# Kernel optimization log

Hardware: AMD Instinct MI355X
Metric: run time of the kernel (lower is better)

## Reference

```python
import jax, jax.numpy as jnp
import numpy as np

MAX_WORDS = 256  # = batch['labels'].shape[1]


def _align(hidden, word_ids, max_words):
    """Batched segment-mean: (B,S,D) subtoken states -> (B,max_words,D) word states.
    Equivalent to align_subtokens_to_words applied per sample (word_ids all valid)."""
    B, S, D = hidden.shape
    seg = (word_ids.astype(jnp.int32) + jnp.arange(B, dtype=jnp.int32)[:, None] * max_words).reshape(-1)
    sums = jax.ops.segment_sum(hidden.reshape(-1, D), seg, num_segments=B * max_words)
    cnts = jax.ops.segment_sum(jnp.ones((B * S,), hidden.dtype), seg, num_segments=B * max_words)
    out = jnp.where(cnts[:, None] > 0, sums / jnp.maximum(cnts, 1.0)[:, None], 0.0)
    return out.reshape(B, max_words, D)


def setup_inputs() -> dict:
    key = jax.random.key(0)
    ks = jax.random.split(key, 8)
    B, S, D, W = 64, 512, 768, MAX_WORDS
    h_hing_sub = jax.random.normal(ks[0], (B, S, D), dtype=jnp.float32)
    h_rob_sub = jax.random.normal(ks[1], (B, S, D), dtype=jnp.float32)
    hing_word_ids = jnp.sort(jax.random.randint(ks[2], (B, S), 0, W), axis=-1).astype(jnp.int32)
    rob_word_ids = jnp.sort(jax.random.randint(ks[3], (B, S), 0, W), axis=-1).astype(jnp.int32)
    num_words = jax.random.randint(ks[4], (B,), 1, W).astype(jnp.int32)
    router_w1 = jax.random.normal(ks[5], (2 * D, 256), dtype=jnp.float32) * (1.0 / np.sqrt(2 * D))
    router_b1 = jnp.zeros((256,), jnp.float32)
    router_w2 = jax.random.normal(ks[6], (256, 1), dtype=jnp.float32) * (1.0 / 16.0)
    router_b2 = jnp.zeros((1,), jnp.float32)
    head_w = jax.random.normal(ks[7], (D, 7), dtype=jnp.float32) * (1.0 / np.sqrt(D))
    head_b = jnp.zeros((7,), jnp.float32)
    return {
        'h_hing_sub': h_hing_sub, 'h_rob_sub': h_rob_sub,
        'hing_word_ids': hing_word_ids, 'rob_word_ids': rob_word_ids,
        'num_words': num_words,
        'router_w1': router_w1, 'router_b1': router_b1,
        'router_w2': router_w2, 'router_b2': router_b2,
        'head_w': head_w, 'head_b': head_b,
    }


def reference(h_hing_sub, h_rob_sub, hing_word_ids, rob_word_ids, num_words,
              router_w1, router_b1, router_w2, router_b2, head_w, head_b):
    W = MAX_WORDS
    # scatter-mean subtokens -> words (the dominant custom-kernel op)
    h_hing = _align(h_hing_sub, hing_word_ids, W)   # (B, W, 768)
    h_rob = _align(h_rob_sub, rob_word_ids, W)      # (B, W, 768)
    # token-level MLP router on concatenated word states (router_input='both')
    router_in = jnp.concatenate([h_hing, h_rob], axis=-1)             # (B, W, 1536)
    hdn = jax.nn.relu(jnp.einsum('bwd,dh->bwh', router_in, router_w1) + router_b1)
    alpha = jax.nn.sigmoid(jnp.einsum('bwh,ho->bwo', hdn, router_w2) + router_b2)  # (B, W, 1)
    blended = alpha * h_hing + (1.0 - alpha) * h_rob                  # (B, W, 768)
    logits = jnp.einsum('bwd,dl->bwl', blended, head_w) + head_b      # (B, W, num_labels)
    l2_disagreement = jnp.linalg.norm(h_hing - h_rob, axis=-1)        # (B, W)
    return logits, alpha.squeeze(-1), l2_disagreement
```

## Files before the change

### kernel.cpp

```cpp
#include <hip/hip_runtime.h>
#include <hip/hip_bf16.h>
#include <math.h>

#define BATCH 64
#define SEQ   512
#define DIM   768
#define NW    256
#define NT    (BATCH * NW)
#define KDIM  1536
#define HID   256
#define NL    7

#define BM  32
#define BK  64
#define BKP 72
#define NKT (KDIM / BK)

typedef __bf16 bf16_t;
typedef bf16_t bf16x4 __attribute__((ext_vector_type(4)));
typedef bf16_t bf16x8 __attribute__((ext_vector_type(8)));
typedef float  f32x4  __attribute__((ext_vector_type(4)));

__global__ __launch_bounds__(256) void prep_kernel(
    const float* __restrict__ w1, bf16_t* __restrict__ w1t,
    const int* __restrict__ idh, const int* __restrict__ idr,
    int* __restrict__ starts)
{
    if (blockIdx.x < 192) {
        int kc = blockIdx.x >> 3;
        int kg = blockIdx.x & 7;
        int n  = threadIdx.x;
        bf16x8 v;
        #pragma unroll
        for (int j = 0; j < 8; j++)
            v[j] = (bf16_t)w1[(size_t)(kc * 64 + kg * 8 + j) * HID + n];
        *(bf16x8*)(w1t + (size_t)kc * (HID * BK) + n * BK + kg * 8) = v;
    } else {
        int blk = blockIdx.x - 192;
        int t = blk >> 6;
        int b = blk & 63;
        const int* ids = (t ? idr : idh) + b * SEQ;
        int w = threadIdx.x;
        int lo = 0, hi = SEQ;
        while (lo < hi) {
            int m = (lo + hi) >> 1;
            if (ids[m] < w) lo = m + 1; else hi = m;
        }
        int* row = starts + blk * 257;
        row[w] = lo;
        if (w == 0) row[256] = SEQ;
    }
}

#define WPT 16
#define CH  8

typedef const __attribute__((address_space(1))) uint32_t g_u32;
typedef __attribute__((address_space(3))) uint32_t lds_u32;

__device__ __forceinline__ void gload_lds16(const float* g, float* l) {
    __builtin_amdgcn_global_load_lds((g_u32*)g, (lds_u32*)l, 16, 0, 0);
}

__global__ __launch_bounds__(256, 2) void align_kernel(
    const float* __restrict__ hh, const float* __restrict__ hr,
    const int* __restrict__ starts, bf16_t* __restrict__ X)
{
    __shared__ float lds[4][CH][256];

    int tid  = threadIdx.x;
    int lane = tid & 63;
    int wv   = tid >> 6;
    int task = blockIdx.x * 4 + wv;
    int dc   = task % 3;
    int q    = task / 3;
    int wb   = q & 15;
    int t    = (q >> 4) & 1;
    int b    = q >> 5;

    const int*   st  = starts + (t * 64 + b) * 257 + wb * WPT;
    const float* src = (t ? hr : hh) + (size_t)b * SEQ * DIM + dc * 256;
    bf16_t*      dst = X + (size_t)b * NW * KDIM + (size_t)wb * WPT * KDIM
                         + t * DIM + dc * 256;
    float*       myl = &lds[wv][0][0];

    bf16x4 zero4 = {};
    int lo = st[0];
    int hi = st[WPT];

    int w  = 0;
    int nb = st[1];
    while (nb == lo) {
        *(bf16x4*)(dst + (size_t)w * KDIM + lane * 4) = zero4;
        w++;
        if (w == WPT) break;
        nb = st[w + 1];
    }

    if (lo < hi) {
        f32x4 acc = {0.f, 0.f, 0.f, 0.f};
        int wstart = lo;

        for (int cs = lo; cs < hi; cs += CH) {
            #pragma unroll
            for (int i = 0; i < CH; i++) {
                int s = cs + i;
                s = s < hi ? s : hi - 1;
                gload_lds16(src + (size_t)s * DIM + lane * 4, myl + i * 256);
            }
            asm volatile("s_waitcnt vmcnt(0)" ::: "memory");

            #pragma unroll
            for (int i = 0; i < CH; i++) {
                int s = cs + i;
                if (s < hi) {
                    f32x4 v = *(const f32x4*)(myl + i * 256 + lane * 4);
                    acc[0] += v[0]; acc[1] += v[1];
                    acc[2] += v[2]; acc[3] += v[3];
                    if (s + 1 == nb) {
                        float invn = 1.0f / (float)(nb - wstart);
                        bf16x4 o;
                        o[0] = (bf16_t)(acc[0] * invn);
                        o[1] = (bf16_t)(acc[1] * invn);
                        o[2] = (bf16_t)(acc[2] * invn);
                        o[3] = (bf16_t)(acc[3] * invn);
                        *(bf16x4*)(dst + (size_t)w * KDIM + lane * 4) = o;
                        acc = (f32x4){0.f, 0.f, 0.f, 0.f};
                        w++; wstart = nb;
                        while (w < WPT) {
                            int nb2 = st[w + 1];
                            if (nb2 > wstart) { nb = nb2; break; }
                            *(bf16x4*)(dst + (size_t)w * KDIM + lane * 4) = zero4;
                            w++;
                        }
                    }
                }
            }
        }
    }
}

__global__ __launch_bounds__(256) void gemm_alpha_kernel(
    const bf16_t* __restrict__ X, const bf16_t* __restrict__ w1t,
    const float* __restrict__ b1, const float* __restrict__ w2,
    const float* __restrict__ b2, float* __restrict__ out)
{
    __shared__ __align__(16) bf16_t Xs[BM][BKP];
    __shared__ __align__(16) bf16_t Ws[HID][BKP];
    __shared__ float alpha_acc[BM];

    int tid   = threadIdx.x;
    int lane  = tid & 63;
    int wv    = tid >> 6;
    int row16 = lane & 15;
    int quad  = lane >> 4;
    int tok0  = blockIdx.x * BM;

    f32x4 acc[2][4];
    #pragma unroll
    for (int mi = 0; mi < 2; mi++)
        #pragma unroll
        for (int ni = 0; ni < 4; ni++)
            acc[mi][ni] = (f32x4){0.f, 0.f, 0.f, 0.f};

    int xr = tid >> 3;
    int xc = tid & 7;

    for (int kc = 0; kc < NKT; kc++) {
        {
            const uint4* src = (const uint4*)(X + (size_t)(tok0 + xr) * KDIM + kc * BK + xc * 8);
            *(uint4*)(&Xs[xr][xc * 8]) = *src;
        }
        {
            const uint4* srcb = (const uint4*)(w1t + (size_t)kc * (HID * BK));
            #pragma unroll
            for (int i = 0; i < 8; i++) {
                int cidx = tid + i * 256;
                *(uint4*)(&Ws[cidx >> 3][(cidx & 7) * 8]) = srcb[cidx];
            }
        }
        __syncthreads();
        #pragma unroll
        for (int kk2 = 0; kk2 < 2; kk2++) {
            bf16x8 af[2], bfg[4];
            #pragma unroll
            for (int mi = 0; mi < 2; mi++)
                af[mi] = *(const bf16x8*)(&Xs[mi * 16 + row16][kk2 * 32 + quad * 8]);
            #pragma unroll
            for (int ni = 0; ni < 4; ni++)
                bfg[ni] = *(const bf16x8*)(&Ws[wv * 64 + ni * 16 + row16][kk2 * 32 + quad * 8]);
            #pragma unroll
            for (int mi = 0; mi < 2; mi++)
                #pragma unroll
                for (int ni = 0; ni < 4; ni++)
                    acc[mi][ni] = __builtin_amdgcn_mfma_f32_16x16x32_bf16(
                        af[mi], bfg[ni], acc[mi][ni], 0, 0, 0);
        }
        __syncthreads();
    }

    float w2v[4], b1v[4];
    #pragma unroll
    for (int ni = 0; ni < 4; ni++) {
        int col = wv * 64 + ni * 16 + row16;
        w2v[ni] = w2[col];
        b1v[ni] = b1[col];
    }
    if (tid < BM) alpha_acc[tid] = 0.f;
    __syncthreads();

    #pragma unroll
    for (int mi = 0; mi < 2; mi++) {
        #pragma unroll
        for (int r = 0; r < 4; r++) {
            float p = 0.f;
            #pragma unroll
            for (int ni = 0; ni < 4; ni++) {
                float v = acc[mi][ni][r] + b1v[ni];
                v = v > 0.f ? v : 0.f;
                p += v * w2v[ni];
            }
            p += __shfl_xor(p, 1);
            p += __shfl_xor(p, 2);
            p += __shfl_xor(p, 4);
            p += __shfl_xor(p, 8);
            if (row16 == 0)
                atomicAdd(&alpha_acc[mi * 16 + quad * 4 + r], p);
        }
    }
    __syncthreads();
    if (tid < BM) {
        float a = 1.f / (1.f + expf(-(alpha_acc[tid] + b2[0])));
        out[(size_t)NT * NL + tok0 + tid] = a;
    }
}

__global__ __launch_bounds__(256) void blend_kernel(
    const bf16_t* __restrict__ X, const float* __restrict__ hw,
    const float* __restrict__ hb, float* __restrict__ out)
{
    __shared__ float hws[NL * DIM];
    int tid  = threadIdx.x;
    int lane = tid & 63;
    int wv   = tid >> 6;

    for (int i = tid; i < DIM * NL; i += 256) {
        int d = i / NL, l = i - d * NL;
        hws[l * DIM + d] = hw[i];
    }
    __syncthreads();

    int g   = lane >> 3;
    int u   = lane & 7;
    int tok = blockIdx.x * 32 + wv * 8 + g;

    float a = out[(size_t)NT * NL + tok];
    const bf16_t* xrow = X + (size_t)tok * KDIM;

    float lg[NL] = {0.f, 0.f, 0.f, 0.f, 0.f, 0.f, 0.f};
    float l2 = 0.f;

    #pragma unroll
    for (int k = 0; k < 12; k++) {
        int d0 = (k * 8 + u) * 8;
        bf16x8 hp = *(const bf16x8*)(xrow + d0);
        bf16x8 rp = *(const bf16x8*)(xrow + DIM + d0);
        float bl[8];
        #pragma unroll
        for (int e = 0; e < 8; e++) {
            float hhv = (float)hp[e];
            float hrv = (float)rp[e];
            float df  = hhv - hrv;
            bl[e] = fmaf(a, df, hrv);
            l2 = fmaf(df, df, l2);
        }
        #pragma unroll
        for (int l = 0; l < NL; l++) {
            f32x4 wA = *(const f32x4*)(&hws[l * DIM + d0]);
            f32x4 wB = *(const f32x4*)(&hws[l * DIM + d0 + 4]);
            lg[l] += bl[0]*wA[0] + bl[1]*wA[1] + bl[2]*wA[2] + bl[3]*wA[3]
                   + bl[4]*wB[0] + bl[5]*wB[1] + bl[6]*wB[2] + bl[7]*wB[3];
        }
    }

    #pragma unroll
    for (int off = 1; off < 8; off <<= 1) {
        #pragma unroll
        for (int l = 0; l < NL; l++) lg[l] += __shfl_xor(lg[l], off);
        l2 += __shfl_xor(l2, off);
    }

    if (u < NL) {
        float v = (u == 0) ? lg[0] : (u == 1) ? lg[1] : (u == 2) ? lg[2]
                : (u == 3) ? lg[3] : (u == 4) ? lg[4] : (u == 5) ? lg[5] : lg[6];
        out[(size_t)tok * NL + u] = v + hb[u];
    } else {
        out[(size_t)NT * NL + NT + tok] = sqrtf(l2);
    }
}

extern "C" void kernel_launch(void* const* d_in, const int* in_sizes, int n_in,
                              void* d_out, int out_size, void* d_ws, size_t ws_size,
                              hipStream_t stream)
{
    const float* hh  = (const float*)d_in[0];
    const float* hr  = (const float*)d_in[1];
    const int*   idh = (const int*)d_in[2];
    const int*   idr = (const int*)d_in[3];
    const float* w1  = (const float*)d_in[5];
    const float* b1  = (const float*)d_in[6];
    const float* w2  = (const float*)d_in[7];
    const float* b2  = (const float*)d_in[8];
    const float* hw  = (const float*)d_in[9];
    const float* hb  = (const float*)d_in[10];
    float* out = (float*)d_out;

    bf16_t* X      = (bf16_t*)d_ws;
    bf16_t* w1t    = X + (size_t)NT * KDIM;
    int*    starts = (int*)(w1t + (size_t)NKT * HID * BK);

    prep_kernel<<<320, 256, 0, stream>>>(w1, w1t, idh, idr, starts);
    align_kernel<<<1536, 256, 0, stream>>>(hh, hr, starts, X);
    gemm_alpha_kernel<<<NT / BM, 256, 0, stream>>>(X, w1t, b1, w2, b2, out);
    blend_kernel<<<512, 256, 0, stream>>>(X, hw, hb, out);
}
```

Measured before the change: 292.4 us.

## Rewrite align kernel as one thread per word-feature chunk with direct loads

Replaces the wave-per-16-word align kernel, which staged rows through LDS via global_load_lds in chunks of 8 with full waitcnt barriers, with a flat kernel. Each thread now owns one 4-float column chunk of one word and sums its subtoken rows straight from global memory. The grid grows from 1536 to 24576 blocks to expose more parallelism and remove the serial chunk-and-wait loop. In exchange each thread runs a short variable-length loop with dependent loads and no explicit prefetching, and the launch carries more block overhead.

```diff
diff --git a/kernel.cpp b/kernel.cpp
--- a/kernel.cpp
+++ b/kernel.cpp
@@ -52,92 +52,42 @@
     }
 }
 
-#define WPT 16
-#define CH  8
-
-typedef const __attribute__((address_space(1))) uint32_t g_u32;
-typedef __attribute__((address_space(3))) uint32_t lds_u32;
-
-__device__ __forceinline__ void gload_lds16(const float* g, float* l) {
-    __builtin_amdgcn_global_load_lds((g_u32*)g, (lds_u32*)l, 16, 0, 0);
-}
-
-__global__ __launch_bounds__(256, 2) void align_kernel(
+__global__ __launch_bounds__(256) void align_kernel(
     const float* __restrict__ hh, const float* __restrict__ hr,
     const int* __restrict__ starts, bf16_t* __restrict__ X)
 {
-    __shared__ float lds[4][CH][256];
-
-    int tid  = threadIdx.x;
-    int lane = tid & 63;
-    int wv   = tid >> 6;
-    int task = blockIdx.x * 4 + wv;
-    int dc   = task % 3;
-    int q    = task / 3;
-    int wb   = q & 15;
-    int t    = (q >> 4) & 1;
-    int b    = q >> 5;
-
-    const int*   st  = starts + (t * 64 + b) * 257 + wb * WPT;
-    const float* src = (t ? hr : hh) + (size_t)b * SEQ * DIM + dc * 256;
-    bf16_t*      dst = X + (size_t)b * NW * KDIM + (size_t)wb * WPT * KDIM
-                         + t * DIM + dc * 256;
-    float*       myl = &lds[wv][0][0];
-
-    bf16x4 zero4 = {};
-    int lo = st[0];
-    int hi = st[WPT];
-
-    int w  = 0;
-    int nb = st[1];
-    while (nb == lo) {
-        *(bf16x4*)(dst + (size_t)w * KDIM + lane * 4) = zero4;
-        w++;
-        if (w == WPT) break;
-        nb = st[w + 1];
-    }
-
-    if (lo < hi) {
-        f32x4 acc = {0.f, 0.f, 0.f, 0.f};
-        int wstart = lo;
-
-        for (int cs = lo; cs < hi; cs += CH) {
-            #pragma unroll
-            for (int i = 0; i < CH; i++) {
-                int s = cs + i;
-                s = s < hi ? s : hi - 1;
-                gload_lds16(src + (size_t)s * DIM + lane * 4, myl + i * 256);
-            }
-            asm volatile("s_waitcnt vmcnt(0)" ::: "memory");
-
-            #pragma unroll
-            for (int i = 0; i < CH; i++) {
-                int s = cs + i;
-                if (s < hi) {
-                    f32x4 v = *(const f32x4*)(myl + i * 256 + lane * 4);
-                    acc[0] += v[0]; acc[1] += v[1];
-                    acc[2] += v[2]; acc[3] += v[3];
-                    if (s + 1 == nb) {
-                        float invn = 1.0f / (float)(nb - wstart);
-                        bf16x4 o;
-                        o[0] = (bf16_t)(acc[0] * invn);
-                        o[1] = (bf16_t)(acc[1] * invn);
-                        o[2] = (bf16_t)(acc[2] * invn);
-                        o[3] = (bf16_t)(acc[3] * invn);
-                        *(bf16x4*)(dst + (size_t)w * KDIM + lane * 4) = o;
-                        acc = (f32x4){0.f, 0.f, 0.f, 0.f};
-                        w++; wstart = nb;
-                        while (w < WPT) {
-                            int nb2 = st[w + 1];
-                            if (nb2 > wstart) { nb = nb2; break; }
-                            *(bf16x4*)(dst + (size_t)w * KDIM + lane * 4) = zero4;
-                            w++;
-                        }
-                    }
-                }
-            }
-        }
-    }
+    int idx  = blockIdx.x * 256 + threadIdx.x;
+    int rest = idx / 192;
+    int c    = idx - rest * 192;
+    rest     = __builtin_amdgcn_readfirstlane(rest);
+    int w    = rest & 255;
+    int t    = (rest >> 8) & 1;
+    int b    = rest >> 9;
+
+    const int* st = starts + (t * 64 + b) * 257;
+    int lo = st[w];
+    int hi = st[w + 1];
+
+    const f32x4* src = (const f32x4*)((t ? hr : hh) + (size_t)b * SEQ * DIM);
+    bf16_t*      dst = X + (size_t)b * NW * KDIM + (size_t)w * KDIM
+                         + t * DIM + c * 4;
+
+    bf16x4 o = {};
+    int n = hi - lo;
+    if (n > 0) {
+        f32x4 acc = src[(size_t)lo * 192 + c];
+        for (int s = lo + 1; s < hi; s++) {
+            f32x4 v = src[(size_t)s * 192 + c];
+            acc[0] += v[0]; acc[1] += v[1];
+            acc[2] += v[2]; acc[3] += v[3];
+        }
+        float inv = 1.0f / (float)n;
+        o[0] = (bf16_t)(acc[0] * inv);
+        o[1] = (bf16_t)(acc[1] * inv);
+        o[2] = (bf16_t)(acc[2] * inv);
+        o[3] = (bf16_t)(acc[3] * inv);
+    }
+    *(bf16x4*)dst = o;
 }
 
 __global__ __launch_bounds__(256) void gemm_alpha_kernel(
@@ -320,7 +270,7 @@
     int*    starts = (int*)(w1t + (size_t)NKT * HID * BK);
 
     prep_kernel<<<320, 256, 0, stream>>>(w1, w1t, idh, idr, starts);
-    align_kernel<<<1536, 256, 0, stream>>>(hh, hr, starts, X);
+    align_kernel<<<24576, 256, 0, stream>>>(hh, hr, starts, X);
     gemm_alpha_kernel<<<NT / BM, 256, 0, stream>>>(X, w1t, b1, w2, b2, out);
     blend_kernel<<<512, 256, 0, stream>>>(X, hw, hb, out);
 }
```

Measured after the change: 279.8 us. 1.04x faster.
